# Kernel optimization log

Hardware: AMD Instinct MI355X
Metric: run time of the kernel (lower is better)

Reference implementation:

```python
import jax, jax.numpy as jnp
import numpy as np

EPS = 1e-5

def conv1x1(x, W, b):
    # x: [B,Cin,H,W], W: [Cout,Cin], b: [Cout]
    return jnp.einsum('bchw,oc->bohw', x, W) + b[None, :, None, None]

def mean_variance_norm(feat):
    # feat: [B,C,H,W]; torch .var(dim=2) is unbiased (ddof=1)
    B, C, H, W = feat.shape
    flat = feat.reshape(B, C, H * W)
    mean = flat.mean(axis=2)[:, :, None, None]
    std = jnp.sqrt(flat.var(axis=2, ddof=1) + EPS)[:, :, None, None]
    return (feat - mean) / std

def setup_inputs() -> dict:
    key = jax.random.key(0)
    ks = jax.random.split(key, 10)
    B, C, H, W = 4, 512, 64, 64
    sc = 0.02
    return {
        'content': jax.random.normal(ks[0], (B, C, H, W), jnp.float32),
        'style': jax.random.normal(ks[1], (B, C, H, W), jnp.float32),
        'content_key': jax.random.normal(ks[2], (B, C, H, W), jnp.float32),
        'style_key': jax.random.normal(ks[3], (B, C, H, W), jnp.float32),
        'Wf': jax.random.normal(ks[4], (C, C), jnp.float32) * sc,
        'bf': jax.random.normal(ks[5], (C,), jnp.float32) * sc,
        'Wg': jax.random.normal(ks[6], (C, C), jnp.float32) * sc,
        'bg': jax.random.normal(ks[7], (C,), jnp.float32) * sc,
        'Wh': jax.random.normal(ks[8], (C, C), jnp.float32) * sc,
        'bh': jax.random.normal(ks[9], (C,), jnp.float32) * sc,
    }

def reference(content, style, content_key, style_key, Wf, bf, Wg, bg, Wh, bh):
    B, C, H, W = content.shape
    F = conv1x1(content_key, Wf, bf)          # [B,Ck,H,W]
    G = conv1x1(style_key, Wg, bg)            # [B,Ck,Hs,Ws]
    Hv = conv1x1(style, Wh, bh)               # [B,C,Hs,Ws]
    Ck = F.shape[1]
    N = H * W
    M = G.shape[2] * G.shape[3]
    Fq = F.reshape(B, Ck, N).transpose(0, 2, 1)        # [B,N,Ck]
    Gk = G.reshape(B, Ck, M)                            # [B,Ck,M]
    style_flat = Hv.reshape(B, C, M).transpose(0, 2, 1)  # [B,M,C]
    S = jax.nn.softmax(jnp.einsum('bnc,bcm->bnm', Fq, Gk), axis=-1)  # [B,N,M]
    mean = jnp.einsum('bnm,bmc->bnc', S, style_flat)                  # [B,N,C]
    second = jnp.einsum('bnm,bmc->bnc', S, style_flat ** 2)
    std = jnp.sqrt(jax.nn.relu(second - mean ** 2))
    mean = mean.reshape(B, H, W, C).transpose(0, 3, 1, 2)
    std = std.reshape(B, H, W, C).transpose(0, 3, 1, 2)
    return std * mean_variance_norm(content) + mean
```

## Files before the change

kernel.cpp:

```cpp
#include <hip/hip_runtime.h>

#define B_ 4
#define C_ 512
#define N_ 4096

typedef unsigned short u16;
typedef _Float16 f16;
typedef f16 f16x8 __attribute__((ext_vector_type(8)));
typedef float f32x4 __attribute__((ext_vector_type(4)));

#define MFMA16(a, b, c) __builtin_amdgcn_mfma_f32_16x16x32_f16(a, b, c, 0, 0, 0)

__device__ __forceinline__ u16 f2h(float f) {
  union { f16 h; u16 u; } x; x.h = (f16)f; return x.u;
}
__device__ __forceinline__ float h2f(u16 v) {
  union { u16 u; f16 h; } x; x.u = v; return (float)x.h;
}
__device__ __forceinline__ f16x8 ldA(const void* p) {
  union { uint4 u; f16x8 v; } x; x.u = *(const uint4*)p; return x.v;
}

__global__ __launch_bounds__(256) void cast_w_kernel(const float* __restrict__ in,
                                                     u16* __restrict__ out, int n) {
  int i = (blockIdx.x * 256 + threadIdx.x) * 4;
  if (i >= n) return;
  float4 v = *(const float4*)(in + i);
  uint2 p;
  p.x = f2h(v.x) | ((unsigned)f2h(v.y) << 16);
  p.y = f2h(v.z) | ((unsigned)f2h(v.w) << 16);
  *(uint2*)(out + i) = p;
}

__global__ __launch_bounds__(256) void transpose_cast_kernel(const float* __restrict__ in,
                                                             u16* __restrict__ out) {
  __shared__ float ld[64][65];
  const int b = blockIdx.z, n0 = blockIdx.x * 64, c0 = blockIdx.y * 64;
  const int t = threadIdx.x;
  {
    const int r = t >> 2, q4 = (t & 3) * 16;
    const float* ip = in + ((size_t)(b * C_ + c0 + r)) * N_ + n0 + q4;
#pragma unroll
    for (int j = 0; j < 4; ++j) {
      float4 v = *(const float4*)(ip + j * 4);
      ld[r][q4 + j * 4 + 0] = v.x; ld[r][q4 + j * 4 + 1] = v.y;
      ld[r][q4 + j * 4 + 2] = v.z; ld[r][q4 + j * 4 + 3] = v.w;
    }
  }
  __syncthreads();
  {
    const int r2 = t >> 2, c16 = (t & 3) * 16;
    unsigned pk[8];
#pragma unroll
    for (int j = 0; j < 8; ++j) {
      unsigned lo = f2h(ld[c16 + j * 2 + 0][r2]);
      unsigned hi = f2h(ld[c16 + j * 2 + 1][r2]);
      pk[j] = lo | (hi << 16);
    }
    u16* op = out + ((size_t)(b * N_ + n0 + r2)) * C_ + c0 + c16;
    *(uint4*)(op + 0) = make_uint4(pk[0], pk[1], pk[2], pk[3]);
    *(uint4*)(op + 8) = make_uint4(pk[4], pk[5], pk[6], pk[7]);
  }
}

__global__ __launch_bounds__(512, 4) void conv_kernel(const u16* __restrict__ Xt,
                                                      const u16* __restrict__ Wb,
                                                      const float* __restrict__ bias,
                                                      u16* __restrict__ Outp,
                                                      u16* __restrict__ OutT) {
  __shared__ char sm[65536];
  const int b = blockIdx.z, n0 = blockIdx.x * 64, o0 = blockIdx.y * 64;
  const int t = threadIdx.x, w = t >> 6, lane = t & 63;
  const int wr = w >> 1, wc = w & 1, l15 = lane & 15, l4 = lane >> 4;
#pragma unroll
  for (int k = 0; k < 8; ++k) {
    int ch = t + k * 512, row = ch >> 6, c16 = ch & 63;
    uint4 xv = *(const uint4*)(Xt + ((size_t)(b * N_ + n0 + row)) * C_ + c16 * 8);
    *(uint4*)(sm + row * 1024 + ((c16 ^ (row & 7)) << 4)) = xv;
  }
  __syncthreads();
  f32x4 acc0 = {0, 0, 0, 0}, acc1 = {0, 0, 0, 0};
  const int arow = wr * 16 + l15;
  const int oA = o0 + wc * 32 + l15, oB = oA + 16;
  const u16* wp0 = Wb + (size_t)oA * C_ + l4 * 8;
  const u16* wp1 = Wb + (size_t)oB * C_ + l4 * 8;
#pragma unroll
  for (int kf = 0; kf < 16; ++kf) {
    f16x8 a = ldA(sm + arow * 1024 + (((kf * 4 + l4) ^ (arow & 7)) << 4));
    f16x8 w0 = ldA(wp0 + kf * 32);
    f16x8 w1 = ldA(wp1 + kf * 32);
    acc0 = MFMA16(a, w0, acc0);
    acc1 = MFMA16(a, w1, acc1);
  }
  const float b0 = bias[oA], b1 = bias[oB];
  if (OutT == nullptr) {
#pragma unroll
    for (int r = 0; r < 4; ++r) {
      int n = n0 + wr * 16 + l4 * 4 + r;
      size_t base = ((size_t)(b * N_ + n)) * C_;
      Outp[base + oA] = f2h(acc0[r] + b0);
      Outp[base + oB] = f2h(acc1[r] + b1);
    }
  } else {
    __syncthreads();
    u16* ldsT = (u16*)sm;
#pragma unroll
    for (int r = 0; r < 4; ++r) {
      int nl = wr * 16 + l4 * 4 + r;
      ldsT[(oA - o0) * 72 + nl] = f2h(acc0[r] + b0);
      ldsT[(oB - o0) * 72 + nl] = f2h(acc1[r] + b1);
    }
    __syncthreads();
    const int orow = t >> 3, n8 = (t & 7) * 8;
    uint4 v = *(const uint4*)&ldsT[orow * 72 + n8];
    *(uint4*)(OutT + ((size_t)(b * C_ + o0 + orow)) * N_ + n0 + n8) = v;
  }
}

#define LQ  0
#define LGV 65536
#define LS  131072
#define LPM 140288
#define LPS 141312

__global__ __launch_bounds__(1024, 4) void attn_dual_kernel(const u16* __restrict__ Ft,
                                                            const u16* __restrict__ Gt,
                                                            const u16* __restrict__ V,
                                                            float* __restrict__ OutM,
                                                            float* __restrict__ OutS) {
  __shared__ char sm[142336];
  char* ldsQ = sm + LQ; char* ldsGV = sm + LGV; char* ldsS = sm + LS;
  float* pmax = (float*)(sm + LPM);
  float* psum = (float*)(sm + LPS);

  const int b = blockIdx.y, n0 = blockIdx.x * 64;
  const int t = threadIdx.x, w = t >> 6, lane = t & 63;
  const int ri = w >> 2, mi = w & 3;
  const int l15 = lane & 15, l4 = lane >> 4;

#pragma unroll
  for (int k = 0; k < 4; ++k) {
    int ch = t + k * 1024, row = ch >> 6, c16 = ch & 63;
    uint4 qv = *(const uint4*)(Ft + ((size_t)(b * N_ + n0 + row)) * C_ + c16 * 8);
    *(uint4*)(ldsQ + row * 1024 + ((c16 ^ (row & 7)) << 4)) = qv;
  }

  f32x4 accM[8], accS[8];
#pragma unroll
  for (int i = 0; i < 8; ++i) { accM[i] = (f32x4){0,0,0,0}; accS[i] = (f32x4){0,0,0,0}; }
  float m_run[4] = {-1e30f, -1e30f, -1e30f, -1e30f};
  float l_run[4] = {0, 0, 0, 0};

  const u16* Vb = V + (size_t)(b * C_) * N_;
  __syncthreads();

  for (int it = 0; it < 64; ++it) {
    const int m0 = it * 64;
#pragma unroll
    for (int k = 0; k < 4; ++k) {
      int ch = t + k * 1024, row = ch >> 6, c16 = ch & 63;
      uint4 gv = *(const uint4*)(Gt + ((size_t)(b * N_ + m0 + row)) * C_ + c16 * 8);
      *(uint4*)(ldsGV + row * 1024 + ((c16 ^ (row & 7)) << 4)) = gv;
    }
    __syncthreads();

    f32x4 s0 = {0, 0, 0, 0};
    {
      const int qrow = ri * 16 + l15;
      const int grow = mi * 16 + l15;
#pragma unroll
      for (int kf = 0; kf < 16; ++kf) {
        f16x8 qf = ldA(ldsQ + qrow * 1024 + (((kf * 4 + l4) ^ (qrow & 7)) << 4));
        f16x8 gf = ldA(ldsGV + grow * 1024 + (((kf * 4 + l4) ^ (grow & 7)) << 4));
        s0 = MFMA16(qf, gf, s0);
      }
    }
    float rmax[4];
#pragma unroll
    for (int r = 0; r < 4; ++r) rmax[r] = s0[r];
#pragma unroll
    for (int off = 1; off < 16; off <<= 1)
#pragma unroll
      for (int r = 0; r < 4; ++r) rmax[r] = fmaxf(rmax[r], __shfl_xor(rmax[r], off));
    if (l15 == 0)
#pragma unroll
      for (int r = 0; r < 4; ++r) pmax[mi * 64 + ri * 16 + l4 * 4 + r] = rmax[r];
    __syncthreads();

    float fac[4], mnew[4], rsum[4];
#pragma unroll
    for (int r = 0; r < 4; ++r) {
      int row = ri * 16 + l4 * 4 + r;
      float mt = fmaxf(fmaxf(pmax[row], pmax[64 + row]),
                       fmaxf(pmax[128 + row], pmax[192 + row]));
      float mn = fmaxf(m_run[r], mt);
      fac[r] = __expf(m_run[r] - mn);
      m_run[r] = mn; mnew[r] = mn;
    }
#pragma unroll
    for (int r = 0; r < 4; ++r) {
      float p0 = __expf(s0[r] - mnew[r]);
      u16 pb0 = f2h(p0);
      rsum[r] = h2f(pb0);
      int row = ri * 16 + l4 * 4 + r;
      int m = mi * 16 + l15;
      *(u16*)(ldsS + row * 144 + m * 2) = pb0;
    }
#pragma unroll
    for (int off = 1; off < 16; off <<= 1)
#pragma unroll
      for (int r = 0; r < 4; ++r) rsum[r] += __shfl_xor(rsum[r], off);
    if (l15 == 0)
#pragma unroll
      for (int r = 0; r < 4; ++r) psum[mi * 64 + ri * 16 + l4 * 4 + r] = rsum[r];

#pragma unroll
    for (int k = 0; k < 4; ++k) {
      int ch = t + k * 1024, c = ch >> 3, sl = ch & 7;
      uint4 vv = *(const uint4*)(Vb + (size_t)c * N_ + m0 + sl * 8);
      *(uint4*)(ldsGV + c * 128 + ((sl ^ (c & 7)) << 4)) = vv;
    }
    __syncthreads();

#pragma unroll
    for (int r = 0; r < 4; ++r) {
      int row = ri * 16 + l4 * 4 + r;
      l_run[r] = l_run[r] * fac[r] +
                 ((psum[row] + psum[64 + row]) + (psum[128 + row] + psum[192 + row]));
    }
    bool nch = true;
#pragma unroll
    for (int r = 0; r < 4; ++r) nch = nch && (fac[r] == 1.0f);
    if (!__all(nch)) {
#pragma unroll
      for (int f = 0; f < 8; ++f)
#pragma unroll
        for (int r = 0; r < 4; ++r) { accM[f][r] *= fac[r]; accS[f][r] *= fac[r]; }
    }
    const int srow = ri * 16 + l15;
    f16x8 a0 = ldA(ldsS + srow * 144 + (0 + l4) * 16);
    f16x8 a1 = ldA(ldsS + srow * 144 + (4 + l4) * 16);
#pragma unroll
    for (int f = 0; f < 8; ++f) {
      const int c = mi * 128 + f * 16 + l15;
      f16x8 v0 = ldA(ldsGV + c * 128 + (((0 + l4) ^ (c & 7)) << 4));
      f16x8 v1 = ldA(ldsGV + c * 128 + (((4 + l4) ^ (c & 7)) << 4));
      accM[f] = MFMA16(a0, v0, accM[f]);
      accM[f] = MFMA16(a1, v1, accM[f]);
      f16x8 w0 = v0 * v0, w1 = v1 * v1;
      accS[f] = MFMA16(a0, w0, accS[f]);
      accS[f] = MFMA16(a1, w1, accS[f]);
    }
    __syncthreads();
  }

  float rl[4];
#pragma unroll
  for (int r = 0; r < 4; ++r) rl[r] = 1.0f / l_run[r];
#pragma unroll
  for (int f = 0; f < 8; ++f) {
    const int c = mi * 128 + f * 16 + l15;
#pragma unroll
    for (int r = 0; r < 4; ++r) {
      int n = n0 + ri * 16 + l4 * 4 + r;
      size_t o = ((size_t)(b * N_ + n)) * C_ + c;
      OutM[o] = accM[f][r] * rl[r];
      OutS[o] = accS[f][r] * rl[r];
    }
  }
}

__global__ __launch_bounds__(256) void stats_kernel(const float* __restrict__ content,
                                                    float* __restrict__ stats) {
  const int c = blockIdx.x, b = blockIdx.y;
  const float4* p = (const float4*)(content + ((size_t)(b * C_ + c)) * N_);
  float s = 0.f, ss = 0.f;
  for (int i = threadIdx.x; i < N_ / 4; i += 256) {
    float4 v = p[i];
    s += v.x + v.y + v.z + v.w;
    ss += v.x * v.x + v.y * v.y + v.z * v.z + v.w * v.w;
  }
#pragma unroll
  for (int off = 32; off; off >>= 1) { s += __shfl_down(s, off); ss += __shfl_down(ss, off); }
  __shared__ float as_[4], ass_[4];
  int w = threadIdx.x >> 6;
  if ((threadIdx.x & 63) == 0) { as_[w] = s; ass_[w] = ss; }
  __syncthreads();
  if (threadIdx.x == 0) {
    float S = as_[0] + as_[1] + as_[2] + as_[3];
    float SS = ass_[0] + ass_[1] + ass_[2] + ass_[3];
    float mu = S * (1.0f / N_);
    float var = (SS - (float)N_ * mu * mu) * (1.0f / (N_ - 1));
    stats[(size_t)(b * C_ + c) * 2 + 0] = mu;
    stats[(size_t)(b * C_ + c) * 2 + 1] = rsqrtf(var + 1e-5f);
  }
}

__global__ __launch_bounds__(256) void combine_kernel(const float* __restrict__ content,
                                                      const float* __restrict__ meanb,
                                                      const float* __restrict__ secb,
                                                      const float* __restrict__ stats,
                                                      float* __restrict__ outp) {
  __shared__ float ldM[64][65], ldS[64][65];
  const int b = blockIdx.z, n0 = blockIdx.x * 64, c0 = blockIdx.y * 64;
  const int t = threadIdx.x;
  {
    const int r = t >> 2, q4 = (t & 3) * 16;
    size_t ib = ((size_t)(b * N_ + n0 + r)) * C_ + c0 + q4;
#pragma unroll
    for (int j = 0; j < 4; ++j) {
      float4 mv = *(const float4*)(meanb + ib + j * 4);
      float4 sv = *(const float4*)(secb + ib + j * 4);
      ldM[r][q4 + j * 4 + 0] = mv.x; ldM[r][q4 + j * 4 + 1] = mv.y;
      ldM[r][q4 + j * 4 + 2] = mv.z; ldM[r][q4 + j * 4 + 3] = mv.w;
      ldS[r][q4 + j * 4 + 0] = sv.x; ldS[r][q4 + j * 4 + 1] = sv.y;
      ldS[r][q4 + j * 4 + 2] = sv.z; ldS[r][q4 + j * 4 + 3] = sv.w;
    }
  }
  __syncthreads();
  const int n4 = (t & 15) * 4, cb = t >> 4;
#pragma unroll
  for (int cc = 0; cc < 4; ++cc) {
    int c_loc = cc * 16 + cb;
    int c = c0 + c_loc;
    float mu = stats[(size_t)(b * C_ + c) * 2 + 0];
    float rs = stats[(size_t)(b * C_ + c) * 2 + 1];
    size_t gb = ((size_t)(b * C_ + c)) * N_ + n0 + n4;
    float4 xv = *(const float4*)(content + gb);
    float4 ov;
    {
      float m0_ = ldM[n4 + 0][c_loc], s0_ = ldS[n4 + 0][c_loc];
      float m1_ = ldM[n4 + 1][c_loc], s1_ = ldS[n4 + 1][c_loc];
      float m2_ = ldM[n4 + 2][c_loc], s2_ = ldS[n4 + 2][c_loc];
      float m3_ = ldM[n4 + 3][c_loc], s3_ = ldS[n4 + 3][c_loc];
      ov.x = sqrtf(fmaxf(s0_ - m0_ * m0_, 0.f)) * ((xv.x - mu) * rs) + m0_;
      ov.y = sqrtf(fmaxf(s1_ - m1_ * m1_, 0.f)) * ((xv.y - mu) * rs) + m1_;
      ov.z = sqrtf(fmaxf(s2_ - m2_ * m2_, 0.f)) * ((xv.z - mu) * rs) + m2_;
      ov.w = sqrtf(fmaxf(s3_ - m3_ * m3_, 0.f)) * ((xv.w - mu) * rs) + m3_;
    }
    *(float4*)(outp + gb) = ov;
  }
}

extern "C" void kernel_launch(void* const* d_in, const int* in_sizes, int n_in,
                              void* d_out, int out_size, void* d_ws, size_t ws_size,
                              hipStream_t stream) {
  (void)in_sizes; (void)n_in; (void)out_size; (void)ws_size;
  const float* content = (const float*)d_in[0];
  const float* style   = (const float*)d_in[1];
  const float* ckey    = (const float*)d_in[2];
  const float* skey    = (const float*)d_in[3];
  const float* Wf = (const float*)d_in[4]; const float* bf_ = (const float*)d_in[5];
  const float* Wg = (const float*)d_in[6]; const float* bg_ = (const float*)d_in[7];
  const float* Wh = (const float*)d_in[8]; const float* bh_ = (const float*)d_in[9];
  float* outp = (float*)d_out;
  char* ws = (char*)d_ws;

  const size_t MB = 1u << 20;
  u16*   Ft    = (u16*)(ws + 0 * MB);
  u16*   Gt    = (u16*)(ws + 16 * MB);
  u16*   Hv    = (u16*)(ws + 32 * MB);
  float* stats = (float*)(ws + 48 * MB);
  u16*   Xt    = (u16*)(ws + 48 * MB);
  float* meanb = (float*)(ws + 64 * MB);
  float* secb  = (float*)(ws + 96 * MB);
  u16*   Wb3   = (u16*)(ws + 80 * MB);
  u16* Wbf = Wb3, *Wbg = Wb3 + 262144, *Wbh = Wb3 + 524288;

  const dim3 gT(64, 8, 4);

  cast_w_kernel<<<256, 256, 0, stream>>>(Wf, Wbf, 262144);
  cast_w_kernel<<<256, 256, 0, stream>>>(Wg, Wbg, 262144);
  cast_w_kernel<<<256, 256, 0, stream>>>(Wh, Wbh, 262144);

  transpose_cast_kernel<<<gT, 256, 0, stream>>>(ckey, Xt);
  conv_kernel<<<gT, 512, 0, stream>>>(Xt, Wbf, bf_, Ft, nullptr);
  transpose_cast_kernel<<<gT, 256, 0, stream>>>(skey, Xt);
  conv_kernel<<<gT, 512, 0, stream>>>(Xt, Wbg, bg_, Gt, nullptr);
  transpose_cast_kernel<<<gT, 256, 0, stream>>>(style, Xt);
  conv_kernel<<<gT, 512, 0, stream>>>(Xt, Wbh, bh_, nullptr, Hv);

  stats_kernel<<<dim3(C_, B_), 256, 0, stream>>>(content, stats);
  attn_dual_kernel<<<dim3(64, B_), 1024, 0, stream>>>(Ft, Gt, Hv, meanb, secb);
  combine_kernel<<<gT, 256, 0, stream>>>(content, meanb, secb, stats, outp);
}
```

Before: 1.016 ms.

## Shrink attention tile to 32x32 with split-K score and per-wave local softmax max

The attention kernel moves from 64-query blocks of 1024 threads to 32-query blocks of 512 threads, which doubles the grid and halves LDS use so more blocks can be resident per CU. The QK^T reduction over channels is split across wave pairs and combined through LDS. Each column-group wave exponentiates against its own local max, and the scale is corrected later by rescaling P with alpha, which removes one barrier between max and exp. Half the waves load V while the others compute softmax. In exchange there are extra LDS round trips, f16 rescaling of P (a small precision risk), and twice as many iterations with a G reload after each one.

```diff
diff --git a/kernel.cpp b/kernel.cpp
--- a/kernel.cpp
+++ b/kernel.cpp
@@ -118,32 +118,44 @@
 }
 
 #define LQ  0
-#define LGV 65536
-#define LS  131072
-#define LPM 140288
-#define LPS 141312
-
-__global__ __launch_bounds__(1024, 4) void attn_dual_kernel(const u16* __restrict__ Ft,
-                                                            const u16* __restrict__ Gt,
-                                                            const u16* __restrict__ V,
-                                                            float* __restrict__ OutM,
-                                                            float* __restrict__ OutS) {
-  __shared__ char sm[142336];
-  char* ldsQ = sm + LQ; char* ldsGV = sm + LGV; char* ldsS = sm + LS;
+#define LGV 32768
+#define LSP 73728
+#define LP  77824
+#define LPM 80384
+#define LPS 80640
+#define LMO 80896
+
+__global__ __launch_bounds__(512, 4) void attn_dual_kernel(const u16* __restrict__ Ft,
+                                                           const u16* __restrict__ Gt,
+                                                           const u16* __restrict__ V,
+                                                           float* __restrict__ OutM,
+                                                           float* __restrict__ OutS) {
+  __shared__ char sm[81152];
+  char* ldsQ = sm + LQ; char* ldsGV = sm + LGV; char* ldsP = sm + LP;
+  float* spart = (float*)(sm + LSP);
   float* pmax = (float*)(sm + LPM);
   float* psum = (float*)(sm + LPS);
-
-  const int b = blockIdx.y, n0 = blockIdx.x * 64;
+  float* mold = (float*)(sm + LMO);
+
+  const int b = blockIdx.y, n0 = blockIdx.x * 32;
   const int t = threadIdx.x, w = t >> 6, lane = t & 63;
-  const int ri = w >> 2, mi = w & 3;
+  const int kh = w & 1, wq = w >> 1, ri = wq >> 1, mi = wq & 1;
   const int l15 = lane & 15, l4 = lane >> 4;
+  const int cjb = ((kh << 1) | mi) * 128;
 
 #pragma unroll
   for (int k = 0; k < 4; ++k) {
-    int ch = t + k * 1024, row = ch >> 6, c16 = ch & 63;
+    int ch = t + k * 512, row = ch >> 6, c16 = ch & 63;
     uint4 qv = *(const uint4*)(Ft + ((size_t)(b * N_ + n0 + row)) * C_ + c16 * 8);
     *(uint4*)(ldsQ + row * 1024 + ((c16 ^ (row & 7)) << 4)) = qv;
   }
+#pragma unroll
+  for (int k = 0; k < 4; ++k) {
+    int ch = t + k * 512, row = ch >> 6, c16 = ch & 63;
+    uint4 gv = *(const uint4*)(Gt + ((size_t)(b * N_ + row)) * C_ + c16 * 8);
+    *(uint4*)(ldsGV + row * 1024 + ((c16 ^ (row & 7)) << 4)) = gv;
+  }
+  if (t < 32) mold[t] = -1e30f;
 
   f32x4 accM[8], accS[8];
 #pragma unroll
@@ -152,81 +164,88 @@
   float l_run[4] = {0, 0, 0, 0};
 
   const u16* Vb = V + (size_t)(b * C_) * N_;
+  const int spb = ((ri << 1) | mi) << 10;
   __syncthreads();
 
-  for (int it = 0; it < 64; ++it) {
-    const int m0 = it * 64;
-#pragma unroll
-    for (int k = 0; k < 4; ++k) {
-      int ch = t + k * 1024, row = ch >> 6, c16 = ch & 63;
-      uint4 gv = *(const uint4*)(Gt + ((size_t)(b * N_ + m0 + row)) * C_ + c16 * 8);
-      *(uint4*)(ldsGV + row * 1024 + ((c16 ^ (row & 7)) << 4)) = gv;
-    }
-    __syncthreads();
-
+  for (int it = 0; it < 128; ++it) {
+    const int m0 = it * 32;
     f32x4 s0 = {0, 0, 0, 0};
     {
       const int qrow = ri * 16 + l15;
       const int grow = mi * 16 + l15;
 #pragma unroll
-      for (int kf = 0; kf < 16; ++kf) {
-        f16x8 qf = ldA(ldsQ + qrow * 1024 + (((kf * 4 + l4) ^ (qrow & 7)) << 4));
-        f16x8 gf = ldA(ldsGV + grow * 1024 + (((kf * 4 + l4) ^ (grow & 7)) << 4));
+      for (int kf = 0; kf < 8; ++kf) {
+        int c16 = (kh << 5) + kf * 4 + l4;
+        f16x8 qf = ldA(ldsQ + qrow * 1024 + ((c16 ^ (qrow & 7)) << 4));
+        f16x8 gf = ldA(ldsGV + grow * 1024 + ((c16 ^ (grow & 7)) << 4));
         s0 = MFMA16(qf, gf, s0);
       }
     }
-    float rmax[4];
-#pragma unroll
-    for (int r = 0; r < 4; ++r) rmax[r] = s0[r];
-#pragma unroll
-    for (int off = 1; off < 16; off <<= 1)
-#pragma unroll
-      for (int r = 0; r < 4; ++r) rmax[r] = fmaxf(rmax[r], __shfl_xor(rmax[r], off));
-    if (l15 == 0)
-#pragma unroll
-      for (int r = 0; r < 4; ++r) pmax[mi * 64 + ri * 16 + l4 * 4 + r] = rmax[r];
-    __syncthreads();
-
-    float fac[4], mnew[4], rsum[4];
+    if (kh) {
+#pragma unroll
+      for (int r = 0; r < 4; ++r)
+        *(float*)((char*)spart + spb + (l4 * 4 + r) * 64 + l15 * 4) = s0[r];
+    }
+    __syncthreads();
+
+    if (!kh) {
+#pragma unroll
+      for (int r = 0; r < 4; ++r)
+        s0[r] += *(const float*)((const char*)spart + spb + (l4 * 4 + r) * 64 + l15 * 4);
+      float mu[4];
+#pragma unroll
+      for (int r = 0; r < 4; ++r) mu[r] = s0[r];
+#pragma unroll
+      for (int off = 1; off < 16; off <<= 1)
+#pragma unroll
+        for (int r = 0; r < 4; ++r) mu[r] = fmaxf(mu[r], __shfl_xor(mu[r], off));
+      float rsum[4];
+#pragma unroll
+      for (int r = 0; r < 4; ++r) {
+        float beta = fmaxf(mu[r], m_run[r]);
+        float p = __expf(s0[r] - beta);
+        u16 pb = f2h(p);
+        rsum[r] = h2f(pb);
+        int row = ri * 16 + l4 * 4 + r;
+        *(u16*)(ldsP + row * 80 + (mi * 16 + l15) * 2) = pb;
+      }
+#pragma unroll
+      for (int off = 1; off < 16; off <<= 1)
+#pragma unroll
+        for (int r = 0; r < 4; ++r) rsum[r] += __shfl_xor(rsum[r], off);
+      if (l15 == 0)
+#pragma unroll
+        for (int r = 0; r < 4; ++r) {
+          int row = ri * 16 + l4 * 4 + r;
+          pmax[mi * 32 + row] = mu[r];
+          psum[mi * 32 + row] = rsum[r];
+        }
+    } else {
+      const int oi = wq * 64 + lane;
+#pragma unroll
+      for (int k = 0; k < 8; ++k) {
+        int ch = oi + k * 256, c = ch >> 2, sl = ch & 3;
+        uint4 vv = *(const uint4*)(Vb + (size_t)c * N_ + m0 + sl * 8);
+        *(uint4*)(ldsGV + c * 80 + sl * 16) = vv;
+      }
+    }
+    __syncthreads();
+
+    const float* moldR = mold + (it & 1) * 32;
+    float* moldW = mold + ((it + 1) & 1) * 32;
+    float fac[4];
 #pragma unroll
     for (int r = 0; r < 4; ++r) {
       int row = ri * 16 + l4 * 4 + r;
-      float mt = fmaxf(fmaxf(pmax[row], pmax[64 + row]),
-                       fmaxf(pmax[128 + row], pmax[192 + row]));
-      float mn = fmaxf(m_run[r], mt);
+      float q0 = pmax[row], q1 = pmax[32 + row];
+      float mn = fmaxf(m_run[r], fmaxf(q0, q1));
       fac[r] = __expf(m_run[r] - mn);
-      m_run[r] = mn; mnew[r] = mn;
-    }
-#pragma unroll
-    for (int r = 0; r < 4; ++r) {
-      float p0 = __expf(s0[r] - mnew[r]);
-      u16 pb0 = f2h(p0);
-      rsum[r] = h2f(pb0);
-      int row = ri * 16 + l4 * 4 + r;
-      int m = mi * 16 + l15;
-      *(u16*)(ldsS + row * 144 + m * 2) = pb0;
-    }
-#pragma unroll
-    for (int off = 1; off < 16; off <<= 1)
-#pragma unroll
-      for (int r = 0; r < 4; ++r) rsum[r] += __shfl_xor(rsum[r], off);
-    if (l15 == 0)
-#pragma unroll
-      for (int r = 0; r < 4; ++r) psum[mi * 64 + ri * 16 + l4 * 4 + r] = rsum[r];
-
-#pragma unroll
-    for (int k = 0; k < 4; ++k) {
-      int ch = t + k * 1024, c = ch >> 3, sl = ch & 7;
-      uint4 vv = *(const uint4*)(Vb + (size_t)c * N_ + m0 + sl * 8);
-      *(uint4*)(ldsGV + c * 128 + ((sl ^ (c & 7)) << 4)) = vv;
-    }
-    __syncthreads();
-
-#pragma unroll
-    for (int r = 0; r < 4; ++r) {
-      int row = ri * 16 + l4 * 4 + r;
-      l_run[r] = l_run[r] * fac[r] +
-                 ((psum[row] + psum[64 + row]) + (psum[128 + row] + psum[192 + row]));
+      float l = l_run[r] * fac[r];
+      l += psum[row]      * __expf(fmaxf(q0, m_run[r]) - mn);
+      l += psum[32 + row] * __expf(fmaxf(q1, m_run[r]) - mn);
+      l_run[r] = l;
+      if (kh == 0 && mi == 0 && l15 == 0) moldW[row] = mn;
+      m_run[r] = mn;
     }
     bool nch = true;
 #pragma unroll
@@ -237,19 +256,35 @@
 #pragma unroll
         for (int r = 0; r < 4; ++r) { accM[f][r] *= fac[r]; accS[f][r] *= fac[r]; }
     }
-    const int srow = ri * 16 + l15;
-    f16x8 a0 = ldA(ldsS + srow * 144 + (0 + l4) * 16);
-    f16x8 a1 = ldA(ldsS + srow * 144 + (4 + l4) * 16);
-#pragma unroll
-    for (int f = 0; f < 8; ++f) {
-      const int c = mi * 128 + f * 16 + l15;
-      f16x8 v0 = ldA(ldsGV + c * 128 + (((0 + l4) ^ (c & 7)) << 4));
-      f16x8 v1 = ldA(ldsGV + c * 128 + (((4 + l4) ^ (c & 7)) << 4));
-      accM[f] = MFMA16(a0, v0, accM[f]);
-      accM[f] = MFMA16(a1, v1, accM[f]);
-      f16x8 w0 = v0 * v0, w1 = v1 * v1;
-      accS[f] = MFMA16(a0, w0, accS[f]);
-      accS[f] = MFMA16(a1, w1, accS[f]);
+
+    {
+      const int arow = ri * 16 + l15;
+      float mo = moldR[arow];
+      float q0a = pmax[arow], q1a = pmax[32 + arow];
+      float mnA = fmaxf(mo, fmaxf(q0a, q1a));
+      float al0 = __expf(fmaxf(q0a, mo) - mnA);
+      float al1 = __expf(fmaxf(q1a, mo) - mnA);
+      float alpha = (l4 < 2) ? al0 : al1;
+      f16x8 a0 = ldA(ldsP + arow * 80 + l4 * 16);
+      a0 = a0 * (f16)alpha;
+#pragma unroll
+      for (int f = 0; f < 8; ++f) {
+        const int c = cjb + f * 16 + l15;
+        f16x8 v0 = ldA(ldsGV + c * 80 + l4 * 16);
+        accM[f] = MFMA16(a0, v0, accM[f]);
+        f16x8 w0 = v0 * v0;
+        accS[f] = MFMA16(a0, w0, accS[f]);
+      }
+    }
+    __syncthreads();
+
+    if (it < 127) {
+#pragma unroll
+      for (int k = 0; k < 4; ++k) {
+        int ch = t + k * 512, row = ch >> 6, c16 = ch & 63;
+        uint4 gv = *(const uint4*)(Gt + ((size_t)(b * N_ + m0 + 32 + row)) * C_ + c16 * 8);
+        *(uint4*)(ldsGV + row * 1024 + ((c16 ^ (row & 7)) << 4)) = gv;
+      }
     }
     __syncthreads();
   }
@@ -259,7 +294,7 @@
   for (int r = 0; r < 4; ++r) rl[r] = 1.0f / l_run[r];
 #pragma unroll
   for (int f = 0; f < 8; ++f) {
-    const int c = mi * 128 + f * 16 + l15;
+    const int c = cjb + f * 16 + l15;
 #pragma unroll
     for (int r = 0; r < 4; ++r) {
       int n = n0 + ri * 16 + l4 * 4 + r;
@@ -381,6 +416,6 @@
   conv_kernel<<<gT, 512, 0, stream>>>(Xt, Wbh, bh_, nullptr, Hv);
 
   stats_kernel<<<dim3(C_, B_), 256, 0, stream>>>(content, stats);
-  attn_dual_kernel<<<dim3(64, B_), 1024, 0, stream>>>(Ft, Gt, Hv, meanb, secb);
+  attn_dual_kernel<<<dim3(128, B_), 512, 0, stream>>>(Ft, Gt, Hv, meanb, secb);
   combine_kernel<<<gT, 256, 0, stream>>>(content, meanb, secb, stats, outp);
 }
```

After: 1.903 ms. 87.3% more time.

## Warp-specialize attention loop: softmax warps, V-loader warps, G-prefetch warps

Applied to the files above, without the earlier changes.

Restructures the fused attention loop into warp-specialized roles. Four waves compute the 64x32 score tile and the full-row softmax (no cross-wave max/sum exchange), eight waves load the V tile, and four waves prefetch the next G tile into registers. All waves then do the PV/PV² MFMAs. The M tile is halved to 32, which doubles the iteration count but cuts barriers per iteration from three to two and overlaps global loads with the QK and softmax work. The cost is that score compute is concentrated on a quarter of the waves, leaving the rest idle during that phase, plus more per-iteration overhead.

```diff
diff --git a/kernel.cpp b/kernel.cpp
--- a/kernel.cpp
+++ b/kernel.cpp
@@ -118,25 +118,26 @@
 }
 
 #define LQ  0
-#define LGV 65536
-#define LS  131072
-#define LPM 140288
-#define LPS 141312
+#define LG  65536
+#define LV  98304
+#define LP  139264
+#define LF  144384
+#define LL  144640
 
 __global__ __launch_bounds__(1024, 4) void attn_dual_kernel(const u16* __restrict__ Ft,
                                                             const u16* __restrict__ Gt,
                                                             const u16* __restrict__ V,
                                                             float* __restrict__ OutM,
                                                             float* __restrict__ OutS) {
-  __shared__ char sm[142336];
-  char* ldsQ = sm + LQ; char* ldsGV = sm + LGV; char* ldsS = sm + LS;
-  float* pmax = (float*)(sm + LPM);
-  float* psum = (float*)(sm + LPS);
+  __shared__ char sm[144896];
+  char* ldsQ = sm + LQ; char* ldsG = sm + LG; char* ldsV = sm + LV; char* ldsP = sm + LP;
+  float* facv = (float*)(sm + LF);
+  float* lbuf = (float*)(sm + LL);
 
   const int b = blockIdx.y, n0 = blockIdx.x * 64;
   const int t = threadIdx.x, w = t >> 6, lane = t & 63;
-  const int ri = w >> 2, mi = w & 3;
   const int l15 = lane & 15, l4 = lane >> 4;
+  const int ri = w >> 2, ci = w & 3;
 
 #pragma unroll
   for (int k = 0; k < 4; ++k) {
@@ -144,6 +145,12 @@
     uint4 qv = *(const uint4*)(Ft + ((size_t)(b * N_ + n0 + row)) * C_ + c16 * 8);
     *(uint4*)(ldsQ + row * 1024 + ((c16 ^ (row & 7)) << 4)) = qv;
   }
+#pragma unroll
+  for (int k = 0; k < 2; ++k) {
+    int ch = t + k * 1024, row = ch >> 6, c16 = ch & 63;
+    uint4 gv = *(const uint4*)(Gt + ((size_t)(b * N_ + row)) * C_ + c16 * 8);
+    *(uint4*)(ldsG + row * 1024 + ((c16 ^ (row & 7)) << 4)) = gv;
+  }
 
   f32x4 accM[8], accS[8];
 #pragma unroll
@@ -154,112 +161,129 @@
   const u16* Vb = V + (size_t)(b * C_) * N_;
   __syncthreads();
 
-  for (int it = 0; it < 64; ++it) {
-    const int m0 = it * 64;
-#pragma unroll
-    for (int k = 0; k < 4; ++k) {
-      int ch = t + k * 1024, row = ch >> 6, c16 = ch & 63;
-      uint4 gv = *(const uint4*)(Gt + ((size_t)(b * N_ + m0 + row)) * C_ + c16 * 8);
-      *(uint4*)(ldsGV + row * 1024 + ((c16 ^ (row & 7)) << 4)) = gv;
+  for (int it = 0; it < 128; ++it) {
+    const int m0 = it * 32;
+    uint4 g0p, g1p, g2p, g3p, g4p, g5p, g6p, g7p;
+
+    if (w < 4) {
+      f32x4 s0 = {0, 0, 0, 0}, s1 = {0, 0, 0, 0};
+      {
+        const int qrow = w * 16 + l15;
+        const int g0r = l15, g1r = 16 + l15;
+#pragma unroll
+        for (int kf = 0; kf < 16; ++kf) {
+          int c16 = kf * 4 + l4;
+          f16x8 qf = ldA(ldsQ + qrow * 1024 + ((c16 ^ (qrow & 7)) << 4));
+          f16x8 ga = ldA(ldsG + g0r * 1024 + ((c16 ^ (g0r & 7)) << 4));
+          f16x8 gb = ldA(ldsG + g1r * 1024 + ((c16 ^ (g1r & 7)) << 4));
+          s0 = MFMA16(qf, ga, s0);
+          s1 = MFMA16(qf, gb, s1);
+        }
+      }
+      float rmax[4];
+#pragma unroll
+      for (int r = 0; r < 4; ++r) rmax[r] = fmaxf(s0[r], s1[r]);
+#pragma unroll
+      for (int off = 1; off < 16; off <<= 1)
+#pragma unroll
+        for (int r = 0; r < 4; ++r) rmax[r] = fmaxf(rmax[r], __shfl_xor(rmax[r], off));
+      float fac0[4], rsum[4];
+#pragma unroll
+      for (int r = 0; r < 4; ++r) {
+        float mn = fmaxf(m_run[r], rmax[r]);
+        fac0[r] = __expf(m_run[r] - mn);
+        float p0 = __expf(s0[r] - mn);
+        float p1 = __expf(s1[r] - mn);
+        u16 pb0 = f2h(p0), pb1 = f2h(p1);
+        rsum[r] = h2f(pb0) + h2f(pb1);
+        int row = w * 16 + l4 * 4 + r;
+        *(u16*)(ldsP + row * 80 + l15 * 2) = pb0;
+        *(u16*)(ldsP + row * 80 + 32 + l15 * 2) = pb1;
+        m_run[r] = mn;
+      }
+#pragma unroll
+      for (int off = 1; off < 16; off <<= 1)
+#pragma unroll
+        for (int r = 0; r < 4; ++r) rsum[r] += __shfl_xor(rsum[r], off);
+      if (l15 == 0)
+#pragma unroll
+        for (int r = 0; r < 4; ++r) {
+          int row = w * 16 + l4 * 4 + r;
+          l_run[r] = l_run[r] * fac0[r] + rsum[r];
+          facv[row] = fac0[r];
+        }
+      else
+#pragma unroll
+        for (int r = 0; r < 4; ++r) l_run[r] = l_run[r] * fac0[r] + rsum[r];
+    } else if (w < 12) {
+      const int t2 = t - 256;
+#pragma unroll
+      for (int k = 0; k < 4; ++k) {
+        int ch = t2 + k * 512, c = ch >> 2, sl = ch & 3;
+        uint4 vv = *(const uint4*)(Vb + (size_t)c * N_ + m0 + sl * 8);
+        *(uint4*)(ldsV + c * 80 + sl * 16) = vv;
+      }
+    } else if (it < 127) {
+      const int t3 = t - 768;
+      const u16* gb_ = Gt + ((size_t)(b * N_ + m0 + 32)) * C_;
+      g0p = *(const uint4*)(gb_ + (((t3 +    0) >> 6)) * C_ + ((t3 +    0) & 63) * 8);
+      g1p = *(const uint4*)(gb_ + (((t3 +  256) >> 6)) * C_ + ((t3 +  256) & 63) * 8);
+      g2p = *(const uint4*)(gb_ + (((t3 +  512) >> 6)) * C_ + ((t3 +  512) & 63) * 8);
+      g3p = *(const uint4*)(gb_ + (((t3 +  768) >> 6)) * C_ + ((t3 +  768) & 63) * 8);
+      g4p = *(const uint4*)(gb_ + (((t3 + 1024) >> 6)) * C_ + ((t3 + 1024) & 63) * 8);
+      g5p = *(const uint4*)(gb_ + (((t3 + 1280) >> 6)) * C_ + ((t3 + 1280) & 63) * 8);
+      g6p = *(const uint4*)(gb_ + (((t3 + 1536) >> 6)) * C_ + ((t3 + 1536) & 63) * 8);
+      g7p = *(const uint4*)(gb_ + (((t3 + 1792) >> 6)) * C_ + ((t3 + 1792) & 63) * 8);
     }
     __syncthreads();
 
-    f32x4 s0 = {0, 0, 0, 0};
+    if (w >= 12 && it < 127) {
+      const int t3 = t - 768;
+#pragma unroll
+      for (int k = 0; k < 8; ++k) {
+        int ch = t3 + k * 256, row = ch >> 6, c16 = ch & 63;
+        uint4 gv = (k == 0) ? g0p : (k == 1) ? g1p : (k == 2) ? g2p : (k == 3) ? g3p
+                 : (k == 4) ? g4p : (k == 5) ? g5p : (k == 6) ? g6p : g7p;
+        *(uint4*)(ldsG + row * 1024 + ((c16 ^ (row & 7)) << 4)) = gv;
+      }
+    }
+    float fr[4];
+#pragma unroll
+    for (int r = 0; r < 4; ++r) fr[r] = facv[ri * 16 + l4 * 4 + r];
+    bool nch = true;
+#pragma unroll
+    for (int r = 0; r < 4; ++r) nch = nch && (fr[r] == 1.0f);
+    if (!__all(nch)) {
+#pragma unroll
+      for (int f = 0; f < 8; ++f)
+#pragma unroll
+        for (int r = 0; r < 4; ++r) { accM[f][r] *= fr[r]; accS[f][r] *= fr[r]; }
+    }
     {
-      const int qrow = ri * 16 + l15;
-      const int grow = mi * 16 + l15;
-#pragma unroll
-      for (int kf = 0; kf < 16; ++kf) {
-        f16x8 qf = ldA(ldsQ + qrow * 1024 + (((kf * 4 + l4) ^ (qrow & 7)) << 4));
-        f16x8 gf = ldA(ldsGV + grow * 1024 + (((kf * 4 + l4) ^ (grow & 7)) << 4));
-        s0 = MFMA16(qf, gf, s0);
+      const int arow = ri * 16 + l15;
+      f16x8 a = ldA(ldsP + arow * 80 + l4 * 16);
+#pragma unroll
+      for (int f = 0; f < 8; ++f) {
+        const int c = ci * 128 + f * 16 + l15;
+        f16x8 v0 = ldA(ldsV + c * 80 + l4 * 16);
+        accM[f] = MFMA16(a, v0, accM[f]);
+        f16x8 w0 = v0 * v0;
+        accS[f] = MFMA16(a, w0, accS[f]);
       }
     }
-    float rmax[4];
-#pragma unroll
-    for (int r = 0; r < 4; ++r) rmax[r] = s0[r];
-#pragma unroll
-    for (int off = 1; off < 16; off <<= 1)
-#pragma unroll
-      for (int r = 0; r < 4; ++r) rmax[r] = fmaxf(rmax[r], __shfl_xor(rmax[r], off));
-    if (l15 == 0)
-#pragma unroll
-      for (int r = 0; r < 4; ++r) pmax[mi * 64 + ri * 16 + l4 * 4 + r] = rmax[r];
     __syncthreads();
-
-    float fac[4], mnew[4], rsum[4];
-#pragma unroll
-    for (int r = 0; r < 4; ++r) {
-      int row = ri * 16 + l4 * 4 + r;
-      float mt = fmaxf(fmaxf(pmax[row], pmax[64 + row]),
-                       fmaxf(pmax[128 + row], pmax[192 + row]));
-      float mn = fmaxf(m_run[r], mt);
-      fac[r] = __expf(m_run[r] - mn);
-      m_run[r] = mn; mnew[r] = mn;
-    }
-#pragma unroll
-    for (int r = 0; r < 4; ++r) {
-      float p0 = __expf(s0[r] - mnew[r]);
-      u16 pb0 = f2h(p0);
-      rsum[r] = h2f(pb0);
-      int row = ri * 16 + l4 * 4 + r;
-      int m = mi * 16 + l15;
-      *(u16*)(ldsS + row * 144 + m * 2) = pb0;
-    }
-#pragma unroll
-    for (int off = 1; off < 16; off <<= 1)
-#pragma unroll
-      for (int r = 0; r < 4; ++r) rsum[r] += __shfl_xor(rsum[r], off);
-    if (l15 == 0)
-#pragma unroll
-      for (int r = 0; r < 4; ++r) psum[mi * 64 + ri * 16 + l4 * 4 + r] = rsum[r];
-
-#pragma unroll
-    for (int k = 0; k < 4; ++k) {
-      int ch = t + k * 1024, c = ch >> 3, sl = ch & 7;
-      uint4 vv = *(const uint4*)(Vb + (size_t)c * N_ + m0 + sl * 8);
-      *(uint4*)(ldsGV + c * 128 + ((sl ^ (c & 7)) << 4)) = vv;
-    }
-    __syncthreads();
-
-#pragma unroll
-    for (int r = 0; r < 4; ++r) {
-      int row = ri * 16 + l4 * 4 + r;
-      l_run[r] = l_run[r] * fac[r] +
-                 ((psum[row] + psum[64 + row]) + (psum[128 + row] + psum[192 + row]));
-    }
-    bool nch = true;
-#pragma unroll
-    for (int r = 0; r < 4; ++r) nch = nch && (fac[r] == 1.0f);
-    if (!__all(nch)) {
-#pragma unroll
-      for (int f = 0; f < 8; ++f)
-#pragma unroll
-        for (int r = 0; r < 4; ++r) { accM[f][r] *= fac[r]; accS[f][r] *= fac[r]; }
-    }
-    const int srow = ri * 16 + l15;
-    f16x8 a0 = ldA(ldsS + srow * 144 + (0 + l4) * 16);
-    f16x8 a1 = ldA(ldsS + srow * 144 + (4 + l4) * 16);
-#pragma unroll
-    for (int f = 0; f < 8; ++f) {
-      const int c = mi * 128 + f * 16 + l15;
-      f16x8 v0 = ldA(ldsGV + c * 128 + (((0 + l4) ^ (c & 7)) << 4));
-      f16x8 v1 = ldA(ldsGV + c * 128 + (((4 + l4) ^ (c & 7)) << 4));
-      accM[f] = MFMA16(a0, v0, accM[f]);
-      accM[f] = MFMA16(a1, v1, accM[f]);
-      f16x8 w0 = v0 * v0, w1 = v1 * v1;
-      accS[f] = MFMA16(a0, w0, accS[f]);
-      accS[f] = MFMA16(a1, w1, accS[f]);
-    }
-    __syncthreads();
-  }
-
+  }
+
+  if (w < 4 && l15 == 0)
+#pragma unroll
+    for (int r = 0; r < 4; ++r) lbuf[w * 16 + l4 * 4 + r] = l_run[r];
+  __syncthreads();
   float rl[4];
 #pragma unroll
-  for (int r = 0; r < 4; ++r) rl[r] = 1.0f / l_run[r];
+  for (int r = 0; r < 4; ++r) rl[r] = 1.0f / lbuf[ri * 16 + l4 * 4 + r];
 #pragma unroll
   for (int f = 0; f < 8; ++f) {
-    const int c = mi * 128 + f * 16 + l15;
+    const int c = ci * 128 + f * 16 + l15;
 #pragma unroll
     for (int r = 0; r < 4; ++r) {
       int n = n0 + ri * 16 + l4 * 4 + r;
```

New measurement: 881.6 us. 13.2% less time.
